# Kernel optimization log

Hardware: AMD Instinct MI355X
Metric: run time of the kernel (lower is better)

The kernel has to match this reference:

```python
import jax, jax.numpy as jnp
import numpy as np

N_HEAD = 16
ROT_DIM = 64  # partial rotary dims (< head_size=128)


def _apply_rope(x, cos, sin):
    # x: [B,H,T,R]; cos/sin: [T,R/2]. LLaMA-style pairwise complex rotation.
    x1 = x[..., 0::2]
    x2 = x[..., 1::2]
    c = cos[None, None, :, :]
    s = sin[None, None, :, :]
    o1 = x1 * c - x2 * s
    o2 = x1 * s + x2 * c
    # interleave back: [..., R/2, 2] -> [..., R]
    out = jnp.stack([o1, o2], axis=-1)
    return out.reshape(x.shape)


def setup_inputs() -> dict:
    key = jax.random.key(0)
    k1, k2, k3 = jax.random.split(key, 3)
    B, T, C = 2, 2048, 2048
    D = C // N_HEAD
    x = jax.random.normal(k1, (B, T, C), dtype=jnp.float32)
    W_attn = jax.random.normal(k2, (C, 3 * C), dtype=jnp.float32) * (1.0 / np.sqrt(C))
    W_proj = jax.random.normal(k3, (C, C), dtype=jnp.float32) * (1.0 / np.sqrt(C))
    # rotary cos/sin tables over ROT_DIM dims
    half = ROT_DIM // 2
    inv_freq = 1.0 / (10000.0 ** (np.arange(0, half, dtype=np.float32) / half))
    t = np.arange(T, dtype=np.float32)
    ang = np.outer(t, inv_freq)  # [T, R/2]
    cos = jnp.asarray(np.cos(ang), dtype=jnp.float32)
    sin = jnp.asarray(np.sin(ang), dtype=jnp.float32)
    return {"x": x, "W_attn": W_attn, "W_proj": W_proj, "cos": cos, "sin": sin}


def reference(x, W_attn, W_proj, cos, sin):
    B, T, C = x.shape
    H = N_HEAD
    D = C // H
    qkv = x @ W_attn  # [B,T,3C]
    q, k, v = jnp.split(qkv, 3, axis=-1)
    # [B,T,C] -> [B,H,T,D]
    q = q.reshape(B, T, H, D).transpose(0, 2, 1, 3)
    k = k.reshape(B, T, H, D).transpose(0, 2, 1, 3)
    v = v.reshape(B, T, H, D).transpose(0, 2, 1, 3)
    # partial RoPE on first ROT_DIM dims
    q = jnp.concatenate([_apply_rope(q[..., :ROT_DIM], cos, sin), q[..., ROT_DIM:]], axis=-1)
    k = jnp.concatenate([_apply_rope(k[..., :ROT_DIM], cos, sin), k[..., ROT_DIM:]], axis=-1)
    # bidirectional SDPA, no mask
    scale = 1.0 / jnp.sqrt(jnp.asarray(D, dtype=x.dtype))
    scores = jnp.einsum("bhqd,bhkd->bhqk", q, k) * scale
    attn = jax.nn.softmax(scores, axis=-1)
    y = jnp.einsum("bhqk,bhkd->bhqd", attn, v)  # [B,H,T,D]
    y = y.transpose(0, 2, 1, 3).reshape(B, T, C)
    return y @ W_proj
```

## Files before the change

kernel.cpp:

```cpp
#include <hip/hip_runtime.h>
#include <stdint.h>

typedef unsigned short u16;
typedef __attribute__((ext_vector_type(8))) short short8;
typedef __attribute__((ext_vector_type(4))) float f32x4;

__device__ __forceinline__ float bf2f(u16 u){
  union { uint32_t i; float f; } v; v.i = ((uint32_t)u) << 16; return v.f;
}
__device__ __forceinline__ u16 f2bf(float f){
  union { float f; uint32_t i; } v; v.f = f;
  uint32_t r = v.i + 0x7FFFu + ((v.i >> 16) & 1u);
  return (u16)(r >> 16);
}

typedef __attribute__((address_space(3))) uint32_t lds_u32;
typedef const __attribute__((address_space(1))) uint32_t gl_u32;
__device__ __forceinline__ void gl_lds16(const void* g, void* lds){
  __builtin_amdgcn_global_load_lds((gl_u32*)g, (lds_u32*)lds, 16, 0, 0);
}

__global__ void cast_f32_bf16(const float* __restrict__ src, u16* __restrict__ dst){
  const int i = blockIdx.x * 256 + threadIdx.x;
  const float4 a = ((const float4*)src)[2 * i];
  const float4 b = ((const float4*)src)[2 * i + 1];
  uint4 o;
  o.x = (uint32_t)f2bf(a.x) | ((uint32_t)f2bf(a.y) << 16);
  o.y = (uint32_t)f2bf(a.z) | ((uint32_t)f2bf(a.w) << 16);
  o.z = (uint32_t)f2bf(b.x) | ((uint32_t)f2bf(b.y) << 16);
  o.w = (uint32_t)f2bf(b.z) | ((uint32_t)f2bf(b.w) << 16);
  ((uint4*)dst)[i] = o;
}

__global__ void transpose_f32_bf16(const float* __restrict__ src, u16* __restrict__ dst,
                                   int R, int C){
  __shared__ u16 tile[32][33];
  const int cb = blockIdx.x * 32, rb = blockIdx.y * 32;
  const int tx = threadIdx.x, ty = threadIdx.y;
  #pragma unroll
  for (int i = 0; i < 32; i += 8)
    tile[ty + i][tx] = f2bf(src[(size_t)(rb + ty + i) * C + cb + tx]);
  __syncthreads();
  #pragma unroll
  for (int i = 0; i < 32; i += 8)
    dst[(size_t)(cb + ty + i) * R + rb + tx] = tile[tx][ty + i];
}

__global__ void transpose_v(const u16* __restrict__ qkv, u16* __restrict__ vT){
  __shared__ u16 tile[32][33];
  const int db = blockIdx.x * 32, tb = blockIdx.y * 32, bh = blockIdx.z;
  const int b = bh >> 4, h = bh & 15;
  const int tx = threadIdx.x, ty = threadIdx.y;
  const u16* src = qkv + (size_t)(b * 2048) * 6144 + 4096 + h * 128;
  #pragma unroll
  for (int i = 0; i < 32; i += 8) tile[ty + i][tx] = src[(size_t)(tb + ty + i) * 6144 + db + tx];
  __syncthreads();
  u16* d = vT + (size_t)bh * 128 * 2048;
  #pragma unroll
  for (int i = 0; i < 32; i += 8) d[(size_t)(db + ty + i) * 2048 + tb + tx] = tile[tx][ty + i];
}

__global__ void rope_qk(const u16* __restrict__ qkv, const float* __restrict__ cosb,
                        const float* __restrict__ sinb, u16* __restrict__ qo,
                        u16* __restrict__ ko){
  const int idx = blockIdx.x * 256 + threadIdx.x;
  const int d2 = idx & 63;
  const int h  = (idx >> 6) & 15;
  const int t  = (idx >> 10) & 2047;
  const int b  = (idx >> 21) & 1;
  const int w  = idx >> 22;
  const int incol = w * 2048 + h * 128 + 2 * d2;
  const uint32_t pair = *(const uint32_t*)(qkv + (size_t)(b * 2048 + t) * 6144 + incol);
  float x1 = bf2f((u16)(pair & 0xffff));
  float x2 = bf2f((u16)(pair >> 16));
  float o1 = x1, o2 = x2;
  if (d2 < 32){
    const float c = cosb[t * 32 + d2];
    const float s = sinb[t * 32 + d2];
    o1 = x1 * c - x2 * s;
    o2 = x1 * s + x2 * c;
  }
  const uint32_t outp = (uint32_t)f2bf(o1) | ((uint32_t)f2bf(o2) << 16);
  u16* dst = w ? ko : qo;
  *(uint32_t*)(dst + ((size_t)(b * 16 + h) * 2048 + t) * 128 + 2 * d2) = outp;
}

template<bool F32OUT>
__global__ __launch_bounds__(256) void gemm_bt(const u16* __restrict__ A,
                                               const u16* __restrict__ Bt,
                                               void* __restrict__ Cv,
                                               int M, int N, int K){
  __shared__ __align__(16) u16 sA[128 * 64];
  __shared__ __align__(16) u16 sB[128 * 64];
  const int tid  = threadIdx.x;
  const int lane = tid & 63, wave = tid >> 6;
  const int quad = lane >> 4, l15 = lane & 15;
  const int wr = wave >> 1, wc = wave & 1;
  const int mb = blockIdx.y * 128, nb = blockIdx.x * 128;

  f32x4 acc[4][4];
  #pragma unroll
  for (int i = 0; i < 4; i++)
    #pragma unroll
    for (int j = 0; j < 4; j++) acc[i][j] = (f32x4)0.0f;

  for (int k0 = 0; k0 < K; k0 += 64){
    const u16* Ab = A + (size_t)mb * K + k0;
    const u16* Bb = Bt + (size_t)nb * K + k0;
    #pragma unroll
    for (int r = 0; r < 4; r++){
      const int idx = r * 256 + tid;
      const int row = idx >> 3, c = idx & 7;
      const int gc = (c ^ (row & 7)) * 8;
      gl_lds16(Ab + (size_t)row * K + gc, (char*)sA + r * 4096 + wave * 1024);
      gl_lds16(Bb + (size_t)row * K + gc, (char*)sB + r * 4096 + wave * 1024);
    }
    __syncthreads();
    #pragma unroll
    for (int ks = 0; ks < 2; ks++){
      short8 af[4], bfr[4];
      #pragma unroll
      for (int i = 0; i < 4; i++){
        const int row = wr * 64 + i * 16 + l15;
        const int ch = (ks * 4 + quad) ^ (l15 & 7);
        af[i] = *(const short8*)((const char*)sA + row * 128 + ch * 16);
      }
      #pragma unroll
      for (int j = 0; j < 4; j++){
        const int row = wc * 64 + j * 16 + l15;
        const int ch = (ks * 4 + quad) ^ (l15 & 7);
        bfr[j] = *(const short8*)((const char*)sB + row * 128 + ch * 16);
      }
      #pragma unroll
      for (int i = 0; i < 4; i++)
        #pragma unroll
        for (int j = 0; j < 4; j++)
          acc[i][j] = __builtin_amdgcn_mfma_f32_16x16x32_bf16(af[i], bfr[j], acc[i][j], 0, 0, 0);
    }
    __syncthreads();
  }
  #pragma unroll
  for (int i = 0; i < 4; i++)
    #pragma unroll
    for (int j = 0; j < 4; j++)
      #pragma unroll
      for (int r = 0; r < 4; r++){
        const int row = mb + wr * 64 + i * 16 + quad * 4 + r;
        const int col = nb + wc * 64 + j * 16 + l15;
        if (F32OUT) ((float*)Cv)[(size_t)row * N + col] = acc[i][j][r];
        else        ((u16*)Cv)[(size_t)row * N + col]   = f2bf(acc[i][j][r]);
      }
}

__device__ __forceinline__ void stage8k(const u16* __restrict__ g, int ldK,
                                        char* lds, int call, int tid){
  const int idx = call * 512 + tid;
  const int row = idx >> 3, c = idx & 7;
  gl_lds16(g + (size_t)row * ldK + ((c ^ (row & 7)) * 8),
           lds + call * 8192 + (tid >> 6) * 1024);
}

template<bool F32OUT>
__global__ __launch_bounds__(512, 2) void gemm256_bt(const u16* __restrict__ A,
                                                     const u16* __restrict__ Bt,
                                                     void* __restrict__ Cv,
                                                     int M, int N, int K){
  __shared__ __align__(16) u16 sA[2 * 256 * 64];
  __shared__ __align__(16) u16 sB[2 * 256 * 64];
  const int tid  = threadIdx.x;
  const int lane = tid & 63, wave = tid >> 6;
  const int quad = lane >> 4, l15 = lane & 15;
  const int wm = wave >> 2, wn = wave & 3;

  const int nx = gridDim.x, ny = gridDim.y;
  const int bid = blockIdx.y * nx + blockIdx.x;
  int row, col;
  if ((nx & 7) == 0){
    const int xcd = bid & 7, c = bid >> 3;
    const int cq = c / ny;
    col = xcd * (nx >> 3) + cq;
    row = c - cq * ny;
  } else { col = bid % nx; row = bid / nx; }
  const int mb = row * 256, nb = col * 256;

  const int NT = K >> 6;
  const u16* Ab = A  + (size_t)mb * K;
  const u16* Bb = Bt + (size_t)nb * K;

  f32x4 acc[8][4];
  #pragma unroll
  for (int i = 0; i < 8; i++)
    #pragma unroll
    for (int n = 0; n < 4; n++) acc[i][n] = (f32x4)0.0f;

  #pragma unroll
  for (int r = 0; r < 4; r++) stage8k(Ab, K, (char*)sA, r, tid);
  #pragma unroll
  for (int r = 0; r < 4; r++) stage8k(Bb, K, (char*)sB, r, tid);
  #pragma unroll
  for (int r = 0; r < 4; r++) stage8k(Bb + 64, K, (char*)sB + 32768, r, tid);
  asm volatile("s_waitcnt vmcnt(4)" ::: "memory");
  __builtin_amdgcn_s_barrier();

  for (int s = 0; s < NT; ++s){
    const int cur = s & 1;
    char* sAc = (char*)sA + cur * 32768;
    char* sBc = (char*)sB + cur * 32768;
    char* sAn = (char*)sA + (cur ^ 1) * 32768;
    const u16* An = Ab + (size_t)(s + 1) * 64;
    const u16* Bn = Bb + (size_t)(s + 2) * 64;
    const bool pfA = (s + 1 < NT), pfB = (s + 2 < NT);

    short8 bq[4][2];
    #pragma unroll
    for (int q = 0; q < 4; q++){
      if (q == 0){
        #pragma unroll
        for (int n = 0; n < 4; n++)
          #pragma unroll
          for (int ks = 0; ks < 2; ks++){
            const int row2 = wn * 64 + n * 16 + l15;
            bq[n][ks] = *(const short8*)(sBc + row2 * 128 +
                                         (((ks * 4 + quad) ^ (l15 & 7)) * 16));
          }
      }
      short8 aq[2][2];
      #pragma unroll
      for (int i = 0; i < 2; i++)
        #pragma unroll
        for (int ks = 0; ks < 2; ks++){
          const int row2 = wm * 128 + (q * 2 + i) * 16 + l15;
          aq[i][ks] = *(const short8*)(sAc + row2 * 128 +
                                       (((ks * 4 + quad) ^ (l15 & 7)) * 16));
        }
      if (q == 0 && pfA){ stage8k(An, K, sAn, 0, tid); stage8k(An, K, sAn, 1, tid); }
      if (q == 1 && pfA){ stage8k(An, K, sAn, 2, tid); stage8k(An, K, sAn, 3, tid); }
      if (q == 2 && pfB){ stage8k(Bn, K, sBc, 0, tid); stage8k(Bn, K, sBc, 1, tid); }
      if (q == 3 && pfB){ stage8k(Bn, K, sBc, 2, tid); stage8k(Bn, K, sBc, 3, tid); }

      __builtin_amdgcn_s_barrier();
      asm volatile("s_waitcnt lgkmcnt(0)" ::: "memory");
      __builtin_amdgcn_s_setprio(1);
      #pragma unroll
      for (int ks = 0; ks < 2; ks++)
        #pragma unroll
        for (int i = 0; i < 2; i++)
          #pragma unroll
          for (int n = 0; n < 4; n++)
            acc[q * 2 + i][n] = __builtin_amdgcn_mfma_f32_16x16x32_bf16(
                aq[i][ks], bq[n][ks], acc[q * 2 + i][n], 0, 0, 0);
      __builtin_amdgcn_s_setprio(0);
      if (q == 3){
        if (pfB)      asm volatile("s_waitcnt vmcnt(4)" ::: "memory");
        else if (pfA) asm volatile("s_waitcnt vmcnt(0)" ::: "memory");
      }
      __builtin_amdgcn_s_barrier();
    }
  }

  #pragma unroll
  for (int i = 0; i < 8; i++)
    #pragma unroll
    for (int n = 0; n < 4; n++)
      #pragma unroll
      for (int r = 0; r < 4; r++){
        const int row2 = mb + wm * 128 + i * 16 + quad * 4 + r;
        const int col2 = nb + wn * 64 + n * 16 + l15;
        if (F32OUT) ((float*)Cv)[(size_t)row2 * N + col2] = acc[i][n][r];
        else        ((u16*)Cv)[(size_t)row2 * N + col2]   = f2bf(acc[i][n][r]);
      }
}

__global__ __launch_bounds__(256, 2) void attn(const u16* __restrict__ q,
                                               const u16* __restrict__ k,
                                               const u16* __restrict__ vT,
                                               u16* __restrict__ y){
  __shared__ __align__(16) u16 bufK[64 * 128];
  __shared__ __align__(16) u16 bufV[128 * 64];
  __shared__ __align__(16) u16 bufP[4 * 32 * 64];
  const int tid  = threadIdx.x;
  const int lane = tid & 63, wave = tid >> 6;
  const int quad = lane >> 4, l15 = lane & 15;
  const int bh = blockIdx.x & 31, qt = blockIdx.x >> 5;
  const u16* qbh = q  + (size_t)bh * 2048 * 128;
  const u16* kbh = k  + (size_t)bh * 2048 * 128;
  const u16* vbh = vT + (size_t)bh * 128 * 2048;
  const float scale2 = 0.12754100060254310f;

  short8 qf[2][4];
  #pragma unroll
  for (int p = 0; p < 2; p++){
    #pragma unroll
    for (int rr = 0; rr < 4; rr++){
      const int idx = rr * 256 + tid;
      const int row = idx >> 4, c = idx & 15;
      gl_lds16(qbh + (size_t)(qt * 128 + p * 64 + row) * 128 + ((c ^ (row & 15)) * 8),
               (char*)bufK + rr * 4096 + wave * 1024);
    }
    __syncthreads();
    if ((wave >> 1) == p){
      const int rbase = (wave & 1) * 32;
      #pragma unroll
      for (int i = 0; i < 2; i++)
        #pragma unroll
        for (int ks = 0; ks < 4; ks++){
          const int row = rbase + i * 16 + l15;
          const int ch = (ks * 4 + quad) ^ l15;
          qf[i][ks] = *(const short8*)((const char*)bufK + row * 256 + ch * 16);
        }
    }
    __syncthreads();
  }

  #pragma unroll
  for (int rr = 0; rr < 4; rr++){
    const int idx = rr * 256 + tid;
    const int row = idx >> 4, c = idx & 15;
    gl_lds16(kbh + (size_t)row * 128 + ((c ^ (row & 15)) * 8),
             (char*)bufK + rr * 4096 + wave * 1024);
  }
  __syncthreads();
  #pragma unroll
  for (int rr = 0; rr < 4; rr++){
    const int idx = rr * 256 + tid;
    const int row = idx >> 3, c = idx & 7;
    gl_lds16(vbh + (size_t)row * 2048 + ((c ^ (row & 7)) * 8),
             (char*)bufV + rr * 4096 + wave * 1024);
  }

  f32x4 o[2][8];
  #pragma unroll
  for (int i = 0; i < 2; i++)
    #pragma unroll
    for (int ds = 0; ds < 8; ds++) o[i][ds] = (f32x4)0.0f;
  float l_[2][4] = {{0,0,0,0},{0,0,0,0}};

  for (int kt = 0; kt < 32; kt++){
    f32x4 s[2][4];
    #pragma unroll
    for (int i = 0; i < 2; i++)
      #pragma unroll
      for (int kv = 0; kv < 4; kv++) s[i][kv] = (f32x4)0.0f;
    #pragma unroll
    for (int ks = 0; ks < 4; ks++){
      short8 bfr[4];
      #pragma unroll
      for (int kv = 0; kv < 4; kv++){
        const int row = kv * 16 + l15;
        const int ch = (ks * 4 + quad) ^ l15;
        bfr[kv] = *(const short8*)((const char*)bufK + row * 256 + ch * 16);
      }
      #pragma unroll
      for (int i = 0; i < 2; i++)
        #pragma unroll
        for (int kv = 0; kv < 4; kv++)
          s[i][kv] = __builtin_amdgcn_mfma_f32_16x16x32_bf16(qf[i][ks], bfr[kv], s[i][kv], 0, 0, 0);
    }

    #pragma unroll
    for (int i = 0; i < 2; i++)
      #pragma unroll
      for (int kv = 0; kv < 4; kv++)
        #pragma unroll
        for (int r = 0; r < 4; r++){
          const float p = exp2f(s[i][kv][r] * scale2);
          s[i][kv][r] = p;
          l_[i][r] += p;
        }

    __syncthreads();

    if (kt < 31){
      #pragma unroll
      for (int rr = 0; rr < 4; rr++){
        const int idx = rr * 256 + tid;
        const int row = idx >> 4, c = idx & 15;
        gl_lds16(kbh + (size_t)((kt + 1) * 64 + row) * 128 + ((c ^ (row & 15)) * 8),
                 (char*)bufK + rr * 4096 + wave * 1024);
      }
    }

    #pragma unroll
    for (int i = 0; i < 2; i++)
      #pragma unroll
      for (int kv = 0; kv < 4; kv++)
        #pragma unroll
        for (int r = 0; r < 4; r++){
          const int row = i * 16 + quad * 4 + r;
          const int col = kv * 16 + l15;
          bufP[wave * 2048 + row * 64 + (((col >> 3) ^ (row & 7)) * 8) + (col & 7)]
            = f2bf(s[i][kv][r]);
        }

    #pragma unroll
    for (int ks = 0; ks < 2; ks++){
      short8 pa[2];
      #pragma unroll
      for (int i = 0; i < 2; i++)
        pa[i] = *(const short8*)((const char*)bufP + wave * 4096 + (i * 16 + l15) * 128 +
                                 (((ks * 4 + quad) ^ (l15 & 7)) * 16));
      short8 vb[8];
      #pragma unroll
      for (int ds = 0; ds < 8; ds++){
        const int row = ds * 16 + l15;
        const int ch = (ks * 4 + quad) ^ (row & 7);
        vb[ds] = *(const short8*)((const char*)bufV + row * 128 + ch * 16);
      }
      #pragma unroll
      for (int ds = 0; ds < 8; ds++)
        #pragma unroll
        for (int i = 0; i < 2; i++)
          o[i][ds] = __builtin_amdgcn_mfma_f32_16x16x32_bf16(pa[i], vb[ds], o[i][ds], 0, 0, 0);
    }

    __syncthreads();

    if (kt < 31){
      #pragma unroll
      for (int rr = 0; rr < 4; rr++){
        const int idx = rr * 256 + tid;
        const int row = idx >> 3, c = idx & 7;
        gl_lds16(vbh + (size_t)row * 2048 + (kt + 1) * 64 + ((c ^ (row & 7)) * 8),
                 (char*)bufV + rr * 4096 + wave * 1024);
      }
    }
  }

  #pragma unroll
  for (int i = 0; i < 2; i++)
    #pragma unroll
    for (int r = 0; r < 4; r++){
      #pragma unroll
      for (int off = 1; off < 16; off <<= 1) l_[i][r] += __shfl_xor(l_[i][r], off);
    }

  const int b = bh >> 4, h = bh & 15;
  float inv[2][4];
  #pragma unroll
  for (int i = 0; i < 2; i++)
    #pragma unroll
    for (int r = 0; r < 4; r++) inv[i][r] = 1.0f / l_[i][r];
  #pragma unroll
  for (int i = 0; i < 2; i++)
    #pragma unroll
    for (int ds = 0; ds < 8; ds++)
      #pragma unroll
      for (int r = 0; r < 4; r++){
        const int t = qt * 128 + wave * 32 + i * 16 + quad * 4 + r;
        const int cc = h * 128 + ds * 16 + l15;
        y[((size_t)(b * 2048 + t)) * 2048 + cc] = f2bf(o[i][ds][r] * inv[i][r]);
      }
}

extern "C" void kernel_launch(void* const* d_in, const int* in_sizes, int n_in,
                              void* d_out, int out_size, void* d_ws, size_t ws_size,
                              hipStream_t stream) {
  const float* x    = (const float*)d_in[0];
  const float* Wa   = (const float*)d_in[1];
  const float* Wp   = (const float*)d_in[2];
  const float* cosb = (const float*)d_in[3];
  const float* sinb = (const float*)d_in[4];
  float* out = (float*)d_out;
  char* ws = (char*)d_ws;

  u16* WaT = (u16*)(ws);
  u16* WpT = (u16*)(ws + 25165824);
  u16* xb  = (u16*)(ws + 33554432);
  u16* qkv = (u16*)(ws + 50331648);
  u16* qb  = (u16*)(ws + 100663296);
  u16* kb  = (u16*)(ws + 117440512);
  u16* vTb = (u16*)(ws + 134217728);
  u16* yb  = (u16*)(ws + 33554432);

  dim3 b32(32, 8, 1);
  transpose_f32_bf16<<<dim3(192, 64, 1), b32, 0, stream>>>(Wa, WaT, 2048, 6144);
  transpose_f32_bf16<<<dim3(64, 64, 1),  b32, 0, stream>>>(Wp, WpT, 2048, 2048);
  cast_f32_bf16<<<4096, 256, 0, stream>>>(x, xb);
  gemm256_bt<false><<<dim3(24, 16, 1), 512, 0, stream>>>(xb, WaT, qkv, 4096, 6144, 2048);
  rope_qk<<<32768, 256, 0, stream>>>(qkv, cosb, sinb, qb, kb);
  transpose_v<<<dim3(4, 64, 32), b32, 0, stream>>>(qkv, vTb);
  attn<<<512, 256, 0, stream>>>(qb, kb, vTb, yb);
  gemm_bt<true><<<dim3(16, 32, 1), 256, 0, stream>>>(yb, WpT, out, 4096, 2048, 2048);
}
```

Baseline: 422.0 us.

## Fuse RoPE and head-major Q/K scatter into the QKV GEMM epilogue

The separate rope_qk kernel is removed. The QKV GEMM epilogue now applies the partial rotary embedding in registers, pairing adjacent columns with a lane shuffle, and writes Q and K straight into head-major [B,H,T,D] layout. V goes to a compact [B*T,C] buffer that the V transpose then reads. This drops one launch and a full read and write of Q and K, at the cost of scattered 2-byte stores and cos/sin loads in the GEMM epilogue.

```diff
diff --git a/kernel.cpp b/kernel.cpp
--- a/kernel.cpp
+++ b/kernel.cpp
@@ -46,43 +46,18 @@
     dst[(size_t)(cb + ty + i) * R + rb + tx] = tile[tx][ty + i];
 }
 
-__global__ void transpose_v(const u16* __restrict__ qkv, u16* __restrict__ vT){
+__global__ void transpose_v(const u16* __restrict__ vbuf, u16* __restrict__ vT){
   __shared__ u16 tile[32][33];
   const int db = blockIdx.x * 32, tb = blockIdx.y * 32, bh = blockIdx.z;
   const int b = bh >> 4, h = bh & 15;
   const int tx = threadIdx.x, ty = threadIdx.y;
-  const u16* src = qkv + (size_t)(b * 2048) * 6144 + 4096 + h * 128;
-  #pragma unroll
-  for (int i = 0; i < 32; i += 8) tile[ty + i][tx] = src[(size_t)(tb + ty + i) * 6144 + db + tx];
+  const u16* src = vbuf + (size_t)(b * 2048) * 2048 + h * 128;
+  #pragma unroll
+  for (int i = 0; i < 32; i += 8) tile[ty + i][tx] = src[(size_t)(tb + ty + i) * 2048 + db + tx];
   __syncthreads();
   u16* d = vT + (size_t)bh * 128 * 2048;
   #pragma unroll
   for (int i = 0; i < 32; i += 8) d[(size_t)(db + ty + i) * 2048 + tb + tx] = tile[tx][ty + i];
-}
-
-__global__ void rope_qk(const u16* __restrict__ qkv, const float* __restrict__ cosb,
-                        const float* __restrict__ sinb, u16* __restrict__ qo,
-                        u16* __restrict__ ko){
-  const int idx = blockIdx.x * 256 + threadIdx.x;
-  const int d2 = idx & 63;
-  const int h  = (idx >> 6) & 15;
-  const int t  = (idx >> 10) & 2047;
-  const int b  = (idx >> 21) & 1;
-  const int w  = idx >> 22;
-  const int incol = w * 2048 + h * 128 + 2 * d2;
-  const uint32_t pair = *(const uint32_t*)(qkv + (size_t)(b * 2048 + t) * 6144 + incol);
-  float x1 = bf2f((u16)(pair & 0xffff));
-  float x2 = bf2f((u16)(pair >> 16));
-  float o1 = x1, o2 = x2;
-  if (d2 < 32){
-    const float c = cosb[t * 32 + d2];
-    const float s = sinb[t * 32 + d2];
-    o1 = x1 * c - x2 * s;
-    o2 = x1 * s + x2 * c;
-  }
-  const uint32_t outp = (uint32_t)f2bf(o1) | ((uint32_t)f2bf(o2) << 16);
-  u16* dst = w ? ko : qo;
-  *(uint32_t*)(dst + ((size_t)(b * 16 + h) * 2048 + t) * 128 + 2 * d2) = outp;
 }
 
 template<bool F32OUT>
@@ -160,11 +135,14 @@
            lds + call * 8192 + (tid >> 6) * 1024);
 }
 
-template<bool F32OUT>
-__global__ __launch_bounds__(512, 2) void gemm256_bt(const u16* __restrict__ A,
-                                                     const u16* __restrict__ Bt,
-                                                     void* __restrict__ Cv,
-                                                     int M, int N, int K){
+__global__ __launch_bounds__(512, 2) void gemm256_qkv(const u16* __restrict__ A,
+                                                      const u16* __restrict__ Bt,
+                                                      u16* __restrict__ qb,
+                                                      u16* __restrict__ kb,
+                                                      u16* __restrict__ vbuf,
+                                                      const float* __restrict__ cosb,
+                                                      const float* __restrict__ sinb,
+                                                      int M, int N, int K){
   __shared__ __align__(16) u16 sA[2 * 256 * 64];
   __shared__ __align__(16) u16 sB[2 * 256 * 64];
   const int tid  = threadIdx.x;
@@ -258,17 +236,43 @@
     }
   }
 
-  #pragma unroll
-  for (int i = 0; i < 8; i++)
-    #pragma unroll
-    for (int n = 0; n < 4; n++)
-      #pragma unroll
-      for (int r = 0; r < 4; r++){
-        const int row2 = mb + wm * 128 + i * 16 + quad * 4 + r;
-        const int col2 = nb + wn * 64 + n * 16 + l15;
-        if (F32OUT) ((float*)Cv)[(size_t)row2 * N + col2] = acc[i][n][r];
-        else        ((u16*)Cv)[(size_t)row2 * N + col2]   = f2bf(acc[i][n][r]);
-      }
+  const int regn = nb >> 11;
+  const int b    = mb >> 11;
+  if (regn < 2){
+    u16* dst = regn ? kb : qb;
+    const int colbase = nb & 2047;
+    const bool dorope = ((wn & 1) == 0);
+    #pragma unroll
+    for (int i = 0; i < 8; i++)
+      #pragma unroll
+      for (int n = 0; n < 4; n++)
+        #pragma unroll
+        for (int r = 0; r < 4; r++){
+          const int t   = (mb + wm * 128 + i * 16 + quad * 4 + r) & 2047;
+          const int col = colbase + wn * 64 + n * 16 + l15;
+          float v = acc[i][n][r];
+          const float p = __shfl_xor(v, 1);
+          if (dorope){
+            const int d2 = (n * 16 + l15) >> 1;
+            const float c = cosb[t * 32 + d2];
+            const float s = sinb[t * 32 + d2];
+            v = v * c + ((l15 & 1) ? p * s : -p * s);
+          }
+          dst[((size_t)(b * 16 + (col >> 7)) * 2048 + t) * 128 + (col & 127)] = f2bf(v);
+        }
+  } else {
+    const int colbase = nb - 4096;
+    #pragma unroll
+    for (int i = 0; i < 8; i++)
+      #pragma unroll
+      for (int n = 0; n < 4; n++)
+        #pragma unroll
+        for (int r = 0; r < 4; r++){
+          const int row2 = mb + wm * 128 + i * 16 + quad * 4 + r;
+          const int col2 = colbase + wn * 64 + n * 16 + l15;
+          vbuf[(size_t)row2 * 2048 + col2] = f2bf(acc[i][n][r]);
+        }
+  }
 }
 
 __global__ __launch_bounds__(256, 2) void attn(const u16* __restrict__ q,
@@ -463,22 +467,22 @@
   float* out = (float*)d_out;
   char* ws = (char*)d_ws;
 
-  u16* WaT = (u16*)(ws);
-  u16* WpT = (u16*)(ws + 25165824);
-  u16* xb  = (u16*)(ws + 33554432);
-  u16* qkv = (u16*)(ws + 50331648);
-  u16* qb  = (u16*)(ws + 100663296);
-  u16* kb  = (u16*)(ws + 117440512);
-  u16* vTb = (u16*)(ws + 134217728);
-  u16* yb  = (u16*)(ws + 33554432);
+  u16* WaT  = (u16*)(ws);
+  u16* WpT  = (u16*)(ws + 25165824);
+  u16* xb   = (u16*)(ws + 33554432);
+  u16* vbuf = (u16*)(ws + 50331648);
+  u16* qb   = (u16*)(ws + 100663296);
+  u16* kb   = (u16*)(ws + 117440512);
+  u16* vTb  = (u16*)(ws + 134217728);
+  u16* yb   = (u16*)(ws + 33554432);
 
   dim3 b32(32, 8, 1);
   transpose_f32_bf16<<<dim3(192, 64, 1), b32, 0, stream>>>(Wa, WaT, 2048, 6144);
   transpose_f32_bf16<<<dim3(64, 64, 1),  b32, 0, stream>>>(Wp, WpT, 2048, 2048);
   cast_f32_bf16<<<4096, 256, 0, stream>>>(x, xb);
-  gemm256_bt<false><<<dim3(24, 16, 1), 512, 0, stream>>>(xb, WaT, qkv, 4096, 6144, 2048);
-  rope_qk<<<32768, 256, 0, stream>>>(qkv, cosb, sinb, qb, kb);
-  transpose_v<<<dim3(4, 64, 32), b32, 0, stream>>>(qkv, vTb);
+  gemm256_qkv<<<dim3(24, 16, 1), 512, 0, stream>>>(xb, WaT, qb, kb, vbuf, cosb, sinb,
+                                                   4096, 6144, 2048);
+  transpose_v<<<dim3(4, 64, 32), b32, 0, stream>>>(vbuf, vTb);
   attn<<<512, 256, 0, stream>>>(qb, kb, vTb, yb);
   gemm_bt<true><<<dim3(16, 32, 1), 256, 0, stream>>>(yb, WpT, out, 4096, 2048, 2048);
 }
```

New measurement: 459.3 us. +8.9%, slower.
